# Optimization experiments

Measured on AMD Instinct MI355X. Metric: run time of the kernel, lower is better.

Reference implementation:

```python
import jax, jax.numpy as jnp
import numpy as np

BATCH, T, N_INP, N_HID = 32, 512, 128, 1024
DT = 0.042
RHO = 0.99
INPUT_SCALING = 1.0
THRESHOLD = 0.5
RESET = 0.0
R_ = 1.0   # resistance
C_ = 1.0   # capacity
P = 0.5
HARMONIC = N_HID * P          # scalar, as in source: n_hid * p
SPIKING = N_HID - HARMONIC    # scalar, as in source


def setup_inputs() -> dict:
    key = jax.random.key(0)
    k1, k2, k3, k4, k5 = jax.random.split(key, 5)
    x = jax.random.normal(k1, (BATCH, T, N_INP), dtype=jnp.float32)
    # input-to-hidden in (0, input_scaling), per torch.rand * input_scaling
    x2h = jax.random.uniform(k2, (N_INP, N_HID), dtype=jnp.float32) * INPUT_SCALING
    # hidden-to-hidden: full topology, rescaled to spectral radius rho
    W = np.asarray(jax.random.uniform(k3, (N_HID, N_HID), minval=-1.0, maxval=1.0))
    sr = float(np.max(np.abs(np.linalg.eigvals(W))))
    h2h = jnp.asarray(W * (RHO / sr), dtype=jnp.float32)
    # gamma/epsilon sampled per-unit from uniform ranges (tuple branch of __init__)
    gamma = jax.random.uniform(k4, (N_HID,), minval=0.5, maxval=1.5, dtype=jnp.float32)
    epsilon = jax.random.uniform(k5, (N_HID,), minval=0.001, maxval=0.01, dtype=jnp.float32)
    bias = jnp.zeros((N_HID,), dtype=jnp.float32)
    return {"x": x, "x2h": x2h, "h2h": h2h, "gamma": gamma, "epsilon": epsilon, "bias": bias}


def reference(x, x2h, h2h, gamma, epsilon, bias):
    B = x.shape[0]
    dtype = x.dtype
    u_decay = 1.0 - R_ * C_ * DT  # u = u + R*C*dt*(-u)

    def step(carry, xt):
        hy, hz, u = carry
        # spiking_osc: threshold, reset, leak
        spike = (u > THRESHOLD).astype(dtype)
        u = jnp.where(spike == 1.0, RESET, u)
        u = u * u_decay
        # coupled-oscillator update
        drive = jnp.tanh(xt @ x2h + hy @ h2h + bias)
        hz = hz + DT * (drive - gamma * hy - (epsilon * (hz * HARMONIC) + u * SPIKING))
        hy = hy + DT * hz
        return (hy, hz, u), (hy, hz, u, spike)

    zeros = jnp.zeros((B, N_HID), dtype=dtype)
    (_, _, _), (hy_t, hz_t, u_t, spk_t) = jax.lax.scan(
        step, (zeros, zeros, zeros), jnp.swapaxes(x, 0, 1)
    )
    # (T, B, H) -> (B, T, H), matching the per-step lists of the original
    tr = lambda a: jnp.swapaxes(a, 0, 1)
    return tr(hy_t), tr(hz_t), tr(u_t), tr(spk_t)
```

## Files before the change

### kernel.cpp

```cpp
#include <hip/hip_runtime.h>
#include <cmath>

constexpr int  Bn  = 32, Tn = 512, NIn = 128, Hn = 1024;
constexpr long long TH  = (long long)Tn * Hn;
constexpr long long BTH = (long long)Bn * TH;
constexpr float DTc  = 0.042f;
constexpr float UDEC = 1.0f - 1.0f * 1.0f * DTc;
constexpr float HARM = 512.0f;
constexpr float SPIK = 512.0f;

__device__ unsigned g_tag[16 * 32 * 16];

__global__ void init_tag() {
    int i = threadIdx.x;
    __hip_atomic_store(&g_tag[i * 16], 0u,
                       __ATOMIC_RELAXED, __HIP_MEMORY_SCOPE_AGENT);
}

__global__ __launch_bounds__(256) void pre_gemm(const float* __restrict__ x,
                                                const float* __restrict__ x2h,
                                                const float* __restrict__ bias,
                                                float* __restrict__ pre) {
    __shared__ float xs[64 * 128];
    __shared__ float ws[128 * 64];
    const int tid = threadIdx.x;
    const int rb  = blockIdx.y * 64;
    const int cb  = blockIdx.x * 64;

#pragma unroll
    for (int i = 0; i < 8; ++i) {
        int idx = i * 1024 + tid * 4;
        int r = idx >> 7, k = idx & 127;
        *(float4*)(&xs[r * 128 + k]) =
            *(const float4*)(&x[(long long)(rb + r) * NIn + k]);
    }
#pragma unroll
    for (int i = 0; i < 8; ++i) {
        int idx = i * 1024 + tid * 4;
        int k = idx >> 6, c = idx & 63;
        *(float4*)(&ws[k * 64 + c]) =
            *(const float4*)(&x2h[(long long)k * Hn + cb + c]);
    }
    __syncthreads();

    const int tx = tid & 15, ty = tid >> 4;
    const int r0 = ty * 4, c0 = tx * 4;
    float acc[4][4] = {};
#pragma unroll 4
    for (int k = 0; k < 128; ++k) {
        float4 bv = *(const float4*)(&ws[k * 64 + c0]);
        float a0 = xs[(r0 + 0) * 128 + k];
        float a1 = xs[(r0 + 1) * 128 + k];
        float a2 = xs[(r0 + 2) * 128 + k];
        float a3 = xs[(r0 + 3) * 128 + k];
        acc[0][0] += a0 * bv.x; acc[0][1] += a0 * bv.y; acc[0][2] += a0 * bv.z; acc[0][3] += a0 * bv.w;
        acc[1][0] += a1 * bv.x; acc[1][1] += a1 * bv.y; acc[1][2] += a1 * bv.z; acc[1][3] += a1 * bv.w;
        acc[2][0] += a2 * bv.x; acc[2][1] += a2 * bv.y; acc[2][2] += a2 * bv.z; acc[2][3] += a2 * bv.w;
        acc[3][0] += a3 * bv.x; acc[3][1] += a3 * bv.y; acc[3][2] += a3 * bv.z; acc[3][3] += a3 * bv.w;
    }
    float4 bb = *(const float4*)(&bias[cb + c0]);
#pragma unroll
    for (int i = 0; i < 4; ++i) {
        float4 o;
        o.x = acc[i][0] + bb.x; o.y = acc[i][1] + bb.y;
        o.z = acc[i][2] + bb.z; o.w = acc[i][3] + bb.w;
        *(float4*)(&pre[(long long)(rb + r0 + i) * Hn + cb + c0]) = o;
    }
}

__global__ __launch_bounds__(256, 2) void ron_loop2(const float* __restrict__ h2h,
                                                    const float* __restrict__ gam,
                                                    const float* __restrict__ eps,
                                                    float* __restrict__ out) {
    extern __shared__ float sm[];
    float* hyl  = sm;
    float* wtb  = sm + 2 * 1028;
    float* part = wtb;

    const int tid = threadIdx.x;
    const int bx  = blockIdx.x;
    const int bg  = ((bx & 7) << 1) | (bx >> 8);
    const int hg  = (bx >> 3) & 31;
    const int c0  = hg * 32;
    const int b0  = bg * 2;
    unsigned* mytag   = &g_tag[(bg * 32 + hg) * 16];
    unsigned* tagbase = &g_tag[bg * 32 * 16];

    float* hy_o = out;
    float* hz_o = out + BTH;
    float* u_o  = out + 2 * BTH;
    float* sp_o = out + 3 * BTH;

    const int ks   = tid & 31;
    const int tile = tid >> 5;

    float4 W[4][8];
#pragma unroll
    for (int ch = 0; ch < 4; ++ch) {
        for (int idx = tid; idx < 8 * 1024; idx += 256) {
            int cc2 = idx & 7, k = idx >> 3;
            wtb[cc2 * 1028 + k] = h2h[(long long)k * Hn + c0 + ch * 8 + cc2];
        }
        __syncthreads();
        if ((tile >> 1) == ch) {
#pragma unroll
            for (int j = 0; j < 4; ++j)
#pragma unroll
                for (int m = 0; m < 8; ++m)
                    W[j][m] = *(const float4*)(wtb + ((tile & 1) * 4 + j) * 1028
                                               + (ks + 32 * m) * 4);
        }
        __syncthreads();
    }

    const float* hp0 = hyl + ks * 4;
    const float* hp1 = hp0 + 1028;
    float* pw = part + (tile * 4) * 33 + ks;

    const int r  = tid & 63;
    const int cc = r & 31;
    const int bb = r >> 5;
    const int b  = b0 + bb;
    const int h  = c0 + cc;
    const float g = gam[h];
    const float e = eps[h];
    float hy = 0.0f, hz = 0.0f, u = 0.0f;

#define D4(dst, hv, wv)                                         \
    dst = fmaf(hv.x, wv.x, dst); dst = fmaf(hv.y, wv.y, dst);   \
    dst = fmaf(hv.z, wv.z, dst); dst = fmaf(hv.w, wv.w, dst)

    for (int t = 0; t < Tn; ++t) {
        float pre_v = 0.0f;
        if (tid < 64)
            pre_v = u_o[(long long)b * TH + (long long)t * Hn + h];

        float acc = 0.0f;
        if (t > 0) {
            const long long base = (long long)b0 * TH + (long long)(t - 1) * Hn + tid;
            float v[8];
#pragma unroll
            for (int i = 0; i < 8; ++i) {
                v[i] = __hip_atomic_load(
                    &hy_o[base + (long long)(i >> 2) * TH + (i & 3) * 256],
                    __ATOMIC_RELAXED, __HIP_MEMORY_SCOPE_AGENT);
            }
#pragma unroll
            for (int i = 0; i < 8; ++i)
                hyl[(i >> 2) * 1028 + (i & 3) * 256 + tid] = v[i];
            __syncthreads();

            float a00 = 0.f, a01 = 0.f, a02 = 0.f, a03 = 0.f;
            float a10 = 0.f, a11 = 0.f, a12 = 0.f, a13 = 0.f;
#pragma unroll
            for (int m = 0; m < 8; ++m) {
                const int o4 = m * 128;
                float4 h0 = *(const float4*)(hp0 + o4);
                float4 h1 = *(const float4*)(hp1 + o4);
                D4(a00, h0, W[0][m]); D4(a01, h0, W[1][m]);
                D4(a02, h0, W[2][m]); D4(a03, h0, W[3][m]);
                D4(a10, h1, W[0][m]); D4(a11, h1, W[1][m]);
                D4(a12, h1, W[2][m]); D4(a13, h1, W[3][m]);
            }

            pw[(0 * 32 + 0) * 33] = a00; pw[(0 * 32 + 1) * 33] = a01;
            pw[(0 * 32 + 2) * 33] = a02; pw[(0 * 32 + 3) * 33] = a03;
            pw[(1 * 32 + 0) * 33] = a10; pw[(1 * 32 + 1) * 33] = a11;
            pw[(1 * 32 + 2) * 33] = a12; pw[(1 * 32 + 3) * 33] = a13;
            __syncthreads();

            if (tid < 64) {
                const float* pr = part + r * 33;
                float s0 = 0.f, s1 = 0.f, s2 = 0.f, s3 = 0.f;
#pragma unroll
                for (int k = 0; k < 32; k += 4) {
                    s0 += pr[k + 0]; s1 += pr[k + 1];
                    s2 += pr[k + 2]; s3 += pr[k + 3];
                }
                acc = (s0 + s1) + (s2 + s3);
            }
        }

        float spike = 0.0f;
        long long o = 0;
        if (tid < 64) {
            spike = (u > 0.5f) ? 1.0f : 0.0f;
            u = (spike == 1.0f) ? 0.0f : u;
            u = u * UDEC;
            float drive = tanhf(acc + pre_v);
            hz = hz + DTc * (drive - g * hy - (e * (hz * HARM) + u * SPIK));
            hy = hy + DTc * hz;
            o = (long long)b * TH + (long long)t * Hn + h;
            __hip_atomic_store(&hy_o[o], hy,
                               __ATOMIC_RELAXED, __HIP_MEMORY_SCOPE_AGENT);
        }

        if (t < Tn - 1) {
            __syncthreads();
            if (tid == 0)
                __hip_atomic_store(mytag, (unsigned)(t + 1),
                                   __ATOMIC_RELAXED, __HIP_MEMORY_SCOPE_AGENT);
        }

        if (tid < 64) {
            hz_o[o] = hz;
            u_o[o]  = u;
            sp_o[o] = spike;
        }

        if (t < Tn - 1) {
            if (tid < 64) {
                const unsigned target = (unsigned)(t + 1);
                const int idx = tid & 31;
                for (;;) {
                    unsigned v = __hip_atomic_load(&tagbase[idx * 16],
                                                   __ATOMIC_RELAXED,
                                                   __HIP_MEMORY_SCOPE_AGENT);
                    if (__ballot(v < target) == 0ull) break;
                    __builtin_amdgcn_s_sleep(1);
                }
            }
            __syncthreads();
        }
    }
#undef D4
}

__global__ __launch_bounds__(256, 1) void ron_loop4(const float* __restrict__ h2h,
                                                    const float* __restrict__ gam,
                                                    const float* __restrict__ eps,
                                                    float* __restrict__ out) {
    extern __shared__ float sm[];
    float* hyl  = sm;
    float* wt   = sm + 4 * 1028;
    float* part = wt;

    const int tid = threadIdx.x;
    const int bx  = blockIdx.x;
    const int bg  = bx & 7;
    const int hg  = bx >> 3;
    const int c0  = hg * 32;
    const int b0  = bg * 4;
    unsigned* mytag   = &g_tag[(bg * 32 + hg) * 16];
    unsigned* tagbase = &g_tag[bg * 32 * 16];

    float* hy_o = out;
    float* hz_o = out + BTH;
    float* u_o  = out + 2 * BTH;
    float* sp_o = out + 3 * BTH;

    for (int idx = tid; idx < 32 * 1024; idx += 256) {
        int cc2 = idx & 31, k = idx >> 5;
        wt[cc2 * 1028 + k] = h2h[(long long)k * Hn + c0 + cc2];
    }
    __syncthreads();

    const int ks   = tid & 31;
    const int tile = tid >> 5;

    float4 W[4][8];
#pragma unroll
    for (int j = 0; j < 4; ++j)
#pragma unroll
        for (int m = 0; m < 8; ++m)
            W[j][m] = *(const float4*)(wt + (tile * 4 + j) * 1028 + (ks + 32 * m) * 4);

    const float* hp0 = hyl + ks * 4;
    const float* hp1 = hp0 + 1028;
    const float* hp2 = hp0 + 2 * 1028;
    const float* hp3 = hp0 + 3 * 1028;
    float* pw = part + (tile * 4) * 33 + ks;

    const int r  = tid & 127;
    const int cc = r & 31;
    const int bb = r >> 5;
    const int b  = b0 + bb;
    const int h  = c0 + cc;
    const float g = gam[h];
    const float e = eps[h];
    float hy = 0.0f, hz = 0.0f, u = 0.0f;

#define D4(dst, hv, wv)                                         \
    dst = fmaf(hv.x, wv.x, dst); dst = fmaf(hv.y, wv.y, dst);   \
    dst = fmaf(hv.z, wv.z, dst); dst = fmaf(hv.w, wv.w, dst)

    for (int t = 0; t < Tn; ++t) {
        float pre_v = 0.0f;
        if (tid < 128)
            pre_v = u_o[(long long)b * TH + (long long)t * Hn + h];

        float acc = 0.0f;
        if (t > 0) {
            const long long base = (long long)b0 * TH + (long long)(t - 1) * Hn + tid;
            float v[16];
#pragma unroll
            for (int i = 0; i < 16; ++i) {
                v[i] = __hip_atomic_load(
                    &hy_o[base + (long long)(i >> 2) * TH + (i & 3) * 256],
                    __ATOMIC_RELAXED, __HIP_MEMORY_SCOPE_AGENT);
            }
#pragma unroll
            for (int i = 0; i < 16; ++i)
                hyl[(i >> 2) * 1028 + (i & 3) * 256 + tid] = v[i];
            __syncthreads();

            float a00 = 0.f, a01 = 0.f, a02 = 0.f, a03 = 0.f;
            float a10 = 0.f, a11 = 0.f, a12 = 0.f, a13 = 0.f;
            float a20 = 0.f, a21 = 0.f, a22 = 0.f, a23 = 0.f;
            float a30 = 0.f, a31 = 0.f, a32 = 0.f, a33 = 0.f;
#pragma unroll
            for (int m = 0; m < 8; ++m) {
                const int o4 = m * 128;
                float4 h0 = *(const float4*)(hp0 + o4);
                float4 h1 = *(const float4*)(hp1 + o4);
                float4 h2 = *(const float4*)(hp2 + o4);
                float4 h3 = *(const float4*)(hp3 + o4);
                D4(a00, h0, W[0][m]); D4(a01, h0, W[1][m]); D4(a02, h0, W[2][m]); D4(a03, h0, W[3][m]);
                D4(a10, h1, W[0][m]); D4(a11, h1, W[1][m]); D4(a12, h1, W[2][m]); D4(a13, h1, W[3][m]);
                D4(a20, h2, W[0][m]); D4(a21, h2, W[1][m]); D4(a22, h2, W[2][m]); D4(a23, h2, W[3][m]);
                D4(a30, h3, W[0][m]); D4(a31, h3, W[1][m]); D4(a32, h3, W[2][m]); D4(a33, h3, W[3][m]);
            }

            pw[(0 * 32 + 0) * 33] = a00; pw[(0 * 32 + 1) * 33] = a01;
            pw[(0 * 32 + 2) * 33] = a02; pw[(0 * 32 + 3) * 33] = a03;
            pw[(1 * 32 + 0) * 33] = a10; pw[(1 * 32 + 1) * 33] = a11;
            pw[(1 * 32 + 2) * 33] = a12; pw[(1 * 32 + 3) * 33] = a13;
            pw[(2 * 32 + 0) * 33] = a20; pw[(2 * 32 + 1) * 33] = a21;
            pw[(2 * 32 + 2) * 33] = a22; pw[(2 * 32 + 3) * 33] = a23;
            pw[(3 * 32 + 0) * 33] = a30; pw[(3 * 32 + 1) * 33] = a31;
            pw[(3 * 32 + 2) * 33] = a32; pw[(3 * 32 + 3) * 33] = a33;
            __syncthreads();

            if (tid < 128) {
                const float* pr = part + r * 33;
                float s0 = 0.f, s1 = 0.f, s2 = 0.f, s3 = 0.f;
#pragma unroll
                for (int k = 0; k < 32; k += 4) {
                    s0 += pr[k + 0]; s1 += pr[k + 1];
                    s2 += pr[k + 2]; s3 += pr[k + 3];
                }
                acc = (s0 + s1) + (s2 + s3);
            }
        }

        float spike = 0.0f;
        long long o = 0;
        if (tid < 128) {
            spike = (u > 0.5f) ? 1.0f : 0.0f;
            u = (spike == 1.0f) ? 0.0f : u;
            u = u * UDEC;
            float drive = tanhf(acc + pre_v);
            hz = hz + DTc * (drive - g * hy - (e * (hz * HARM) + u * SPIK));
            hy = hy + DTc * hz;
            o = (long long)b * TH + (long long)t * Hn + h;
            __hip_atomic_store(&hy_o[o], hy,
                               __ATOMIC_RELAXED, __HIP_MEMORY_SCOPE_AGENT);
        }

        if (t < Tn - 1) {
            __syncthreads();
            if (tid == 0)
                __hip_atomic_store(mytag, (unsigned)(t + 1),
                                   __ATOMIC_RELAXED, __HIP_MEMORY_SCOPE_AGENT);
        }

        if (tid < 128) {
            hz_o[o] = hz;
            u_o[o]  = u;
            sp_o[o] = spike;
        }

        if (t < Tn - 1) {
            if (tid < 64) {
                const unsigned target = (unsigned)(t + 1);
                const int idx = tid & 31;
                for (;;) {
                    unsigned v = __hip_atomic_load(&tagbase[idx * 16],
                                                   __ATOMIC_RELAXED,
                                                   __HIP_MEMORY_SCOPE_AGENT);
                    if (__ballot(v < target) == 0ull) break;
                    __builtin_amdgcn_s_sleep(1);
                }
            }
            __syncthreads();
        }
    }
#undef D4
}

extern "C" void kernel_launch(void* const* d_in, const int* in_sizes, int n_in,
                              void* d_out, int out_size, void* d_ws, size_t ws_size,
                              hipStream_t stream) {
    const float* x    = (const float*)d_in[0];
    const float* x2h  = (const float*)d_in[1];
    const float* h2h  = (const float*)d_in[2];
    const float* gam  = (const float*)d_in[3];
    const float* eps  = (const float*)d_in[4];
    const float* bias = (const float*)d_in[5];
    float* out = (float*)d_out;
    float* pre = out + 2 * BTH;

    init_tag<<<1, 512, 0, stream>>>();
    pre_gemm<<<dim3(16, 256), dim3(256), 0, stream>>>(x, x2h, bias, pre);

    const unsigned smem2 = (2 * 1028 + 8 * 1028) * sizeof(float);
    const unsigned smem4 = (4 * 1028 + 32 * 1028) * sizeof(float);
    (void)hipFuncSetAttribute((const void*)ron_loop2,
                              hipFuncAttributeMaxDynamicSharedMemorySize,
                              (int)smem2);
    (void)hipFuncSetAttribute((const void*)ron_loop4,
                              hipFuncAttributeMaxDynamicSharedMemorySize,
                              (int)smem4);

    void* args[] = {(void*)&h2h, (void*)&gam, (void*)&eps, (void*)&out};

    int maxb = 0;
    hipError_t qe = hipOccupancyMaxActiveBlocksPerMultiprocessor(
        &maxb, (const void*)ron_loop2, 256, (size_t)smem2);

    bool launched = false;
    if (qe == hipSuccess && maxb >= 2) {
        launched = (hipLaunchCooperativeKernel((void*)ron_loop2, dim3(512),
                                               dim3(256), args, smem2,
                                               stream) == hipSuccess);
    }
    if (!launched) {
        (void)hipLaunchCooperativeKernel((void*)ron_loop4, dim3(256),
                                         dim3(256), args, smem4, stream);
    }
}
```

Baseline: 1.953 ms.

## Replace two-batch 512-block recurrence with 512-thread four-batch blocks splitting K

Removes the ron_loop2 variant (512 blocks of 256 threads, 2 batches each) and adds ron_loop8, which runs 256 blocks of 512 threads, each covering 4 batches and 32 hidden units. The K dimension is split 64 ways instead of 32, so each thread keeps half as many weights in registers and does half the FMAs per step, at the cost of a longer 64-way shared-memory reduction. Fewer blocks means fewer participants in the per-step flag barrier. The spin-wait in the new kernel also drops the s_sleep, which cuts polling latency but adds memory traffic.

```diff
diff --git a/kernel.cpp b/kernel.cpp
--- a/kernel.cpp
+++ b/kernel.cpp
@@ -68,165 +68,7 @@
     }
 }
 
-__global__ __launch_bounds__(256, 2) void ron_loop2(const float* __restrict__ h2h,
-                                                    const float* __restrict__ gam,
-                                                    const float* __restrict__ eps,
-                                                    float* __restrict__ out) {
-    extern __shared__ float sm[];
-    float* hyl  = sm;
-    float* wtb  = sm + 2 * 1028;
-    float* part = wtb;
-
-    const int tid = threadIdx.x;
-    const int bx  = blockIdx.x;
-    const int bg  = ((bx & 7) << 1) | (bx >> 8);
-    const int hg  = (bx >> 3) & 31;
-    const int c0  = hg * 32;
-    const int b0  = bg * 2;
-    unsigned* mytag   = &g_tag[(bg * 32 + hg) * 16];
-    unsigned* tagbase = &g_tag[bg * 32 * 16];
-
-    float* hy_o = out;
-    float* hz_o = out + BTH;
-    float* u_o  = out + 2 * BTH;
-    float* sp_o = out + 3 * BTH;
-
-    const int ks   = tid & 31;
-    const int tile = tid >> 5;
-
-    float4 W[4][8];
-#pragma unroll
-    for (int ch = 0; ch < 4; ++ch) {
-        for (int idx = tid; idx < 8 * 1024; idx += 256) {
-            int cc2 = idx & 7, k = idx >> 3;
-            wtb[cc2 * 1028 + k] = h2h[(long long)k * Hn + c0 + ch * 8 + cc2];
-        }
-        __syncthreads();
-        if ((tile >> 1) == ch) {
-#pragma unroll
-            for (int j = 0; j < 4; ++j)
-#pragma unroll
-                for (int m = 0; m < 8; ++m)
-                    W[j][m] = *(const float4*)(wtb + ((tile & 1) * 4 + j) * 1028
-                                               + (ks + 32 * m) * 4);
-        }
-        __syncthreads();
-    }
-
-    const float* hp0 = hyl + ks * 4;
-    const float* hp1 = hp0 + 1028;
-    float* pw = part + (tile * 4) * 33 + ks;
-
-    const int r  = tid & 63;
-    const int cc = r & 31;
-    const int bb = r >> 5;
-    const int b  = b0 + bb;
-    const int h  = c0 + cc;
-    const float g = gam[h];
-    const float e = eps[h];
-    float hy = 0.0f, hz = 0.0f, u = 0.0f;
-
-#define D4(dst, hv, wv)                                         \
-    dst = fmaf(hv.x, wv.x, dst); dst = fmaf(hv.y, wv.y, dst);   \
-    dst = fmaf(hv.z, wv.z, dst); dst = fmaf(hv.w, wv.w, dst)
-
-    for (int t = 0; t < Tn; ++t) {
-        float pre_v = 0.0f;
-        if (tid < 64)
-            pre_v = u_o[(long long)b * TH + (long long)t * Hn + h];
-
-        float acc = 0.0f;
-        if (t > 0) {
-            const long long base = (long long)b0 * TH + (long long)(t - 1) * Hn + tid;
-            float v[8];
-#pragma unroll
-            for (int i = 0; i < 8; ++i) {
-                v[i] = __hip_atomic_load(
-                    &hy_o[base + (long long)(i >> 2) * TH + (i & 3) * 256],
-                    __ATOMIC_RELAXED, __HIP_MEMORY_SCOPE_AGENT);
-            }
-#pragma unroll
-            for (int i = 0; i < 8; ++i)
-                hyl[(i >> 2) * 1028 + (i & 3) * 256 + tid] = v[i];
-            __syncthreads();
-
-            float a00 = 0.f, a01 = 0.f, a02 = 0.f, a03 = 0.f;
-            float a10 = 0.f, a11 = 0.f, a12 = 0.f, a13 = 0.f;
-#pragma unroll
-            for (int m = 0; m < 8; ++m) {
-                const int o4 = m * 128;
-                float4 h0 = *(const float4*)(hp0 + o4);
-                float4 h1 = *(const float4*)(hp1 + o4);
-                D4(a00, h0, W[0][m]); D4(a01, h0, W[1][m]);
-                D4(a02, h0, W[2][m]); D4(a03, h0, W[3][m]);
-                D4(a10, h1, W[0][m]); D4(a11, h1, W[1][m]);
-                D4(a12, h1, W[2][m]); D4(a13, h1, W[3][m]);
-            }
-
-            pw[(0 * 32 + 0) * 33] = a00; pw[(0 * 32 + 1) * 33] = a01;
-            pw[(0 * 32 + 2) * 33] = a02; pw[(0 * 32 + 3) * 33] = a03;
-            pw[(1 * 32 + 0) * 33] = a10; pw[(1 * 32 + 1) * 33] = a11;
-            pw[(1 * 32 + 2) * 33] = a12; pw[(1 * 32 + 3) * 33] = a13;
-            __syncthreads();
-
-            if (tid < 64) {
-                const float* pr = part + r * 33;
-                float s0 = 0.f, s1 = 0.f, s2 = 0.f, s3 = 0.f;
-#pragma unroll
-                for (int k = 0; k < 32; k += 4) {
-                    s0 += pr[k + 0]; s1 += pr[k + 1];
-                    s2 += pr[k + 2]; s3 += pr[k + 3];
-                }
-                acc = (s0 + s1) + (s2 + s3);
-            }
-        }
-
-        float spike = 0.0f;
-        long long o = 0;
-        if (tid < 64) {
-            spike = (u > 0.5f) ? 1.0f : 0.0f;
-            u = (spike == 1.0f) ? 0.0f : u;
-            u = u * UDEC;
-            float drive = tanhf(acc + pre_v);
-            hz = hz + DTc * (drive - g * hy - (e * (hz * HARM) + u * SPIK));
-            hy = hy + DTc * hz;
-            o = (long long)b * TH + (long long)t * Hn + h;
-            __hip_atomic_store(&hy_o[o], hy,
-                               __ATOMIC_RELAXED, __HIP_MEMORY_SCOPE_AGENT);
-        }
-
-        if (t < Tn - 1) {
-            __syncthreads();
-            if (tid == 0)
-                __hip_atomic_store(mytag, (unsigned)(t + 1),
-                                   __ATOMIC_RELAXED, __HIP_MEMORY_SCOPE_AGENT);
-        }
-
-        if (tid < 64) {
-            hz_o[o] = hz;
-            u_o[o]  = u;
-            sp_o[o] = spike;
-        }
-
-        if (t < Tn - 1) {
-            if (tid < 64) {
-                const unsigned target = (unsigned)(t + 1);
-                const int idx = tid & 31;
-                for (;;) {
-                    unsigned v = __hip_atomic_load(&tagbase[idx * 16],
-                                                   __ATOMIC_RELAXED,
-                                                   __HIP_MEMORY_SCOPE_AGENT);
-                    if (__ballot(v < target) == 0ull) break;
-                    __builtin_amdgcn_s_sleep(1);
-                }
-            }
-            __syncthreads();
-        }
-    }
-#undef D4
-}
-
-__global__ __launch_bounds__(256, 1) void ron_loop4(const float* __restrict__ h2h,
+__global__ __launch_bounds__(512, 1) void ron_loop8(const float* __restrict__ h2h,
                                                     const float* __restrict__ gam,
                                                     const float* __restrict__ eps,
                                                     float* __restrict__ out) {
@@ -249,27 +91,27 @@
     float* u_o  = out + 2 * BTH;
     float* sp_o = out + 3 * BTH;
 
-    for (int idx = tid; idx < 32 * 1024; idx += 256) {
+    for (int idx = tid; idx < 32 * 1024; idx += 512) {
         int cc2 = idx & 31, k = idx >> 5;
         wt[cc2 * 1028 + k] = h2h[(long long)k * Hn + c0 + cc2];
     }
     __syncthreads();
 
-    const int ks   = tid & 31;
-    const int tile = tid >> 5;
-
-    float4 W[4][8];
+    const int ks   = tid & 63;
+    const int tile = tid >> 6;
+
+    float4 W[4][4];
 #pragma unroll
     for (int j = 0; j < 4; ++j)
 #pragma unroll
-        for (int m = 0; m < 8; ++m)
-            W[j][m] = *(const float4*)(wt + (tile * 4 + j) * 1028 + (ks + 32 * m) * 4);
+        for (int m = 0; m < 4; ++m)
+            W[j][m] = *(const float4*)(wt + (tile * 4 + j) * 1028 + m * 256 + ks * 4);
 
     const float* hp0 = hyl + ks * 4;
     const float* hp1 = hp0 + 1028;
     const float* hp2 = hp0 + 2 * 1028;
     const float* hp3 = hp0 + 3 * 1028;
-    float* pw = part + (tile * 4) * 33 + ks;
+    float* pw = part + (tile * 4) * 65 + ks;
 
     const int r  = tid & 127;
     const int cc = r & 31;
@@ -292,16 +134,16 @@
         float acc = 0.0f;
         if (t > 0) {
             const long long base = (long long)b0 * TH + (long long)(t - 1) * Hn + tid;
-            float v[16];
-#pragma unroll
-            for (int i = 0; i < 16; ++i) {
+            float v[8];
+#pragma unroll
+            for (int i = 0; i < 8; ++i) {
                 v[i] = __hip_atomic_load(
-                    &hy_o[base + (long long)(i >> 2) * TH + (i & 3) * 256],
+                    &hy_o[base + (long long)(i >> 1) * TH + (i & 1) * 512],
                     __ATOMIC_RELAXED, __HIP_MEMORY_SCOPE_AGENT);
             }
 #pragma unroll
-            for (int i = 0; i < 16; ++i)
-                hyl[(i >> 2) * 1028 + (i & 3) * 256 + tid] = v[i];
+            for (int i = 0; i < 8; ++i)
+                hyl[(i >> 1) * 1028 + (i & 1) * 512 + tid] = v[i];
             __syncthreads();
 
             float a00 = 0.f, a01 = 0.f, a02 = 0.f, a03 = 0.f;
@@ -309,8 +151,8 @@
             float a20 = 0.f, a21 = 0.f, a22 = 0.f, a23 = 0.f;
             float a30 = 0.f, a31 = 0.f, a32 = 0.f, a33 = 0.f;
 #pragma unroll
-            for (int m = 0; m < 8; ++m) {
-                const int o4 = m * 128;
+            for (int m = 0; m < 4; ++m) {
+                const int o4 = m * 256;
                 float4 h0 = *(const float4*)(hp0 + o4);
                 float4 h1 = *(const float4*)(hp1 + o4);
                 float4 h2 = *(const float4*)(hp2 + o4);
@@ -321,21 +163,21 @@
                 D4(a30, h3, W[0][m]); D4(a31, h3, W[1][m]); D4(a32, h3, W[2][m]); D4(a33, h3, W[3][m]);
             }
 
-            pw[(0 * 32 + 0) * 33] = a00; pw[(0 * 32 + 1) * 33] = a01;
-            pw[(0 * 32 + 2) * 33] = a02; pw[(0 * 32 + 3) * 33] = a03;
-            pw[(1 * 32 + 0) * 33] = a10; pw[(1 * 32 + 1) * 33] = a11;
-            pw[(1 * 32 + 2) * 33] = a12; pw[(1 * 32 + 3) * 33] = a13;
-            pw[(2 * 32 + 0) * 33] = a20; pw[(2 * 32 + 1) * 33] = a21;
-            pw[(2 * 32 + 2) * 33] = a22; pw[(2 * 32 + 3) * 33] = a23;
-            pw[(3 * 32 + 0) * 33] = a30; pw[(3 * 32 + 1) * 33] = a31;
-            pw[(3 * 32 + 2) * 33] = a32; pw[(3 * 32 + 3) * 33] = a33;
+            pw[(0 * 32 + 0) * 65] = a00; pw[(0 * 32 + 1) * 65] = a01;
+            pw[(0 * 32 + 2) * 65] = a02; pw[(0 * 32 + 3) * 65] = a03;
+            pw[(1 * 32 + 0) * 65] = a10; pw[(1 * 32 + 1) * 65] = a11;
+            pw[(1 * 32 + 2) * 65] = a12; pw[(1 * 32 + 3) * 65] = a13;
+            pw[(2 * 32 + 0) * 65] = a20; pw[(2 * 32 + 1) * 65] = a21;
+            pw[(2 * 32 + 2) * 65] = a22; pw[(2 * 32 + 3) * 65] = a23;
+            pw[(3 * 32 + 0) * 65] = a30; pw[(3 * 32 + 1) * 65] = a31;
+            pw[(3 * 32 + 2) * 65] = a32; pw[(3 * 32 + 3) * 65] = a33;
             __syncthreads();
 
             if (tid < 128) {
-                const float* pr = part + r * 33;
+                const float* pr = part + r * 65;
                 float s0 = 0.f, s1 = 0.f, s2 = 0.f, s3 = 0.f;
 #pragma unroll
-                for (int k = 0; k < 32; k += 4) {
+                for (int k = 0; k < 64; k += 4) {
                     s0 += pr[k + 0]; s1 += pr[k + 1];
                     s2 += pr[k + 2]; s3 += pr[k + 3];
                 }
@@ -379,6 +221,167 @@
                                                    __ATOMIC_RELAXED,
                                                    __HIP_MEMORY_SCOPE_AGENT);
                     if (__ballot(v < target) == 0ull) break;
+                }
+            }
+            __syncthreads();
+        }
+    }
+#undef D4
+}
+
+__global__ __launch_bounds__(256, 1) void ron_loop4(const float* __restrict__ h2h,
+                                                    const float* __restrict__ gam,
+                                                    const float* __restrict__ eps,
+                                                    float* __restrict__ out) {
+    extern __shared__ float sm[];
+    float* hyl  = sm;
+    float* wt   = sm + 4 * 1028;
+    float* part = wt;
+
+    const int tid = threadIdx.x;
+    const int bx  = blockIdx.x;
+    const int bg  = bx & 7;
+    const int hg  = bx >> 3;
+    const int c0  = hg * 32;
+    const int b0  = bg * 4;
+    unsigned* mytag   = &g_tag[(bg * 32 + hg) * 16];
+    unsigned* tagbase = &g_tag[bg * 32 * 16];
+
+    float* hy_o = out;
+    float* hz_o = out + BTH;
+    float* u_o  = out + 2 * BTH;
+    float* sp_o = out + 3 * BTH;
+
+    for (int idx = tid; idx < 32 * 1024; idx += 256) {
+        int cc2 = idx & 31, k = idx >> 5;
+        wt[cc2 * 1028 + k] = h2h[(long long)k * Hn + c0 + cc2];
+    }
+    __syncthreads();
+
+    const int ks   = tid & 31;
+    const int tile = tid >> 5;
+
+    float4 W[4][8];
+#pragma unroll
+    for (int j = 0; j < 4; ++j)
+#pragma unroll
+        for (int m = 0; m < 8; ++m)
+            W[j][m] = *(const float4*)(wt + (tile * 4 + j) * 1028 + (ks + 32 * m) * 4);
+
+    const float* hp0 = hyl + ks * 4;
+    const float* hp1 = hp0 + 1028;
+    const float* hp2 = hp0 + 2 * 1028;
+    const float* hp3 = hp0 + 3 * 1028;
+    float* pw = part + (tile * 4) * 33 + ks;
+
+    const int r  = tid & 127;
+    const int cc = r & 31;
+    const int bb = r >> 5;
+    const int b  = b0 + bb;
+    const int h  = c0 + cc;
+    const float g = gam[h];
+    const float e = eps[h];
+    float hy = 0.0f, hz = 0.0f, u = 0.0f;
+
+#define D4(dst, hv, wv)                                         \
+    dst = fmaf(hv.x, wv.x, dst); dst = fmaf(hv.y, wv.y, dst);   \
+    dst = fmaf(hv.z, wv.z, dst); dst = fmaf(hv.w, wv.w, dst)
+
+    for (int t = 0; t < Tn; ++t) {
+        float pre_v = 0.0f;
+        if (tid < 128)
+            pre_v = u_o[(long long)b * TH + (long long)t * Hn + h];
+
+        float acc = 0.0f;
+        if (t > 0) {
+            const long long base = (long long)b0 * TH + (long long)(t - 1) * Hn + tid;
+            float v[16];
+#pragma unroll
+            for (int i = 0; i < 16; ++i) {
+                v[i] = __hip_atomic_load(
+                    &hy_o[base + (long long)(i >> 2) * TH + (i & 3) * 256],
+                    __ATOMIC_RELAXED, __HIP_MEMORY_SCOPE_AGENT);
+            }
+#pragma unroll
+            for (int i = 0; i < 16; ++i)
+                hyl[(i >> 2) * 1028 + (i & 3) * 256 + tid] = v[i];
+            __syncthreads();
+
+            float a00 = 0.f, a01 = 0.f, a02 = 0.f, a03 = 0.f;
+            float a10 = 0.f, a11 = 0.f, a12 = 0.f, a13 = 0.f;
+            float a20 = 0.f, a21 = 0.f, a22 = 0.f, a23 = 0.f;
+            float a30 = 0.f, a31 = 0.f, a32 = 0.f, a33 = 0.f;
+#pragma unroll
+            for (int m = 0; m < 8; ++m) {
+                const int o4 = m * 128;
+                float4 h0 = *(const float4*)(hp0 + o4);
+                float4 h1 = *(const float4*)(hp1 + o4);
+                float4 h2 = *(const float4*)(hp2 + o4);
+                float4 h3 = *(const float4*)(hp3 + o4);
+                D4(a00, h0, W[0][m]); D4(a01, h0, W[1][m]); D4(a02, h0, W[2][m]); D4(a03, h0, W[3][m]);
+                D4(a10, h1, W[0][m]); D4(a11, h1, W[1][m]); D4(a12, h1, W[2][m]); D4(a13, h1, W[3][m]);
+                D4(a20, h2, W[0][m]); D4(a21, h2, W[1][m]); D4(a22, h2, W[2][m]); D4(a23, h2, W[3][m]);
+                D4(a30, h3, W[0][m]); D4(a31, h3, W[1][m]); D4(a32, h3, W[2][m]); D4(a33, h3, W[3][m]);
+            }
+
+            pw[(0 * 32 + 0) * 33] = a00; pw[(0 * 32 + 1) * 33] = a01;
+            pw[(0 * 32 + 2) * 33] = a02; pw[(0 * 32 + 3) * 33] = a03;
+            pw[(1 * 32 + 0) * 33] = a10; pw[(1 * 32 + 1) * 33] = a11;
+            pw[(1 * 32 + 2) * 33] = a12; pw[(1 * 32 + 3) * 33] = a13;
+            pw[(2 * 32 + 0) * 33] = a20; pw[(2 * 32 + 1) * 33] = a21;
+            pw[(2 * 32 + 2) * 33] = a22; pw[(2 * 32 + 3) * 33] = a23;
+            pw[(3 * 32 + 0) * 33] = a30; pw[(3 * 32 + 1) * 33] = a31;
+            pw[(3 * 32 + 2) * 33] = a32; pw[(3 * 32 + 3) * 33] = a33;
+            __syncthreads();
+
+            if (tid < 128) {
+                const float* pr = part + r * 33;
+                float s0 = 0.f, s1 = 0.f, s2 = 0.f, s3 = 0.f;
+#pragma unroll
+                for (int k = 0; k < 32; k += 4) {
+                    s0 += pr[k + 0]; s1 += pr[k + 1];
+                    s2 += pr[k + 2]; s3 += pr[k + 3];
+                }
+                acc = (s0 + s1) + (s2 + s3);
+            }
+        }
+
+        float spike = 0.0f;
+        long long o = 0;
+        if (tid < 128) {
+            spike = (u > 0.5f) ? 1.0f : 0.0f;
+            u = (spike == 1.0f) ? 0.0f : u;
+            u = u * UDEC;
+            float drive = tanhf(acc + pre_v);
+            hz = hz + DTc * (drive - g * hy - (e * (hz * HARM) + u * SPIK));
+            hy = hy + DTc * hz;
+            o = (long long)b * TH + (long long)t * Hn + h;
+            __hip_atomic_store(&hy_o[o], hy,
+                               __ATOMIC_RELAXED, __HIP_MEMORY_SCOPE_AGENT);
+        }
+
+        if (t < Tn - 1) {
+            __syncthreads();
+            if (tid == 0)
+                __hip_atomic_store(mytag, (unsigned)(t + 1),
+                                   __ATOMIC_RELAXED, __HIP_MEMORY_SCOPE_AGENT);
+        }
+
+        if (tid < 128) {
+            hz_o[o] = hz;
+            u_o[o]  = u;
+            sp_o[o] = spike;
+        }
+
+        if (t < Tn - 1) {
+            if (tid < 64) {
+                const unsigned target = (unsigned)(t + 1);
+                const int idx = tid & 31;
+                for (;;) {
+                    unsigned v = __hip_atomic_load(&tagbase[idx * 16],
+                                                   __ATOMIC_RELAXED,
+                                                   __HIP_MEMORY_SCOPE_AGENT);
+                    if (__ballot(v < target) == 0ull) break;
                     __builtin_amdgcn_s_sleep(1);
                 }
             }
@@ -403,29 +406,21 @@
     init_tag<<<1, 512, 0, stream>>>();
     pre_gemm<<<dim3(16, 256), dim3(256), 0, stream>>>(x, x2h, bias, pre);
 
-    const unsigned smem2 = (2 * 1028 + 8 * 1028) * sizeof(float);
-    const unsigned smem4 = (4 * 1028 + 32 * 1028) * sizeof(float);
-    (void)hipFuncSetAttribute((const void*)ron_loop2,
+    const unsigned smem = (4 * 1028 + 32 * 1028) * sizeof(float);
+    (void)hipFuncSetAttribute((const void*)ron_loop8,
                               hipFuncAttributeMaxDynamicSharedMemorySize,
-                              (int)smem2);
+                              (int)smem);
     (void)hipFuncSetAttribute((const void*)ron_loop4,
                               hipFuncAttributeMaxDynamicSharedMemorySize,
-                              (int)smem4);
+                              (int)smem);
 
     void* args[] = {(void*)&h2h, (void*)&gam, (void*)&eps, (void*)&out};
 
-    int maxb = 0;
-    hipError_t qe = hipOccupancyMaxActiveBlocksPerMultiprocessor(
-        &maxb, (const void*)ron_loop2, 256, (size_t)smem2);
-
-    bool launched = false;
-    if (qe == hipSuccess && maxb >= 2) {
-        launched = (hipLaunchCooperativeKernel((void*)ron_loop2, dim3(512),
-                                               dim3(256), args, smem2,
-                                               stream) == hipSuccess);
-    }
+    bool launched =
+        (hipLaunchCooperativeKernel((void*)ron_loop8, dim3(256), dim3(512),
+                                    args, smem, stream) == hipSuccess);
     if (!launched) {
         (void)hipLaunchCooperativeKernel((void*)ron_loop4, dim3(256),
-                                         dim3(256), args, smem4, stream);
+                                         dim3(256), args, smem, stream);
     }
 }
```

Result: no change. 1.961 ms (+0.4%).
